# Performance work log

Measured on AMD Instinct MI355X. Metric: run time of the kernel, lower is better.

The kernel has to match this reference:

```python
import jax, jax.numpy as jnp
import numpy as np

T, H, I, E, TOPK = 4096, 1024, 2048, 8, 2
RENORMALIZE = True


def setup_inputs() -> dict:
    key = jax.random.key(0)
    k1, k2, k3, k4 = jax.random.split(key, 4)
    x = jax.random.normal(k1, (T, H), dtype=jnp.float32)
    router_logits = jax.random.normal(k2, (T, E), dtype=jnp.float32)
    # w13 stacks [gate; up] projections: [E, 2*I, H]; w2: [E, H, I]
    w13_weight = jax.random.normal(k3, (E, 2 * I, H), dtype=jnp.float32) * 0.02
    w2_weight = jax.random.normal(k4, (E, H, I), dtype=jnp.float32) * 0.02
    return {
        "x": x,
        "router_logits": router_logits,
        "w13_weight": w13_weight,
        "w2_weight": w2_weight,
        "top_k": TOPK,
    }


def reference(x, router_logits, w13_weight, w2_weight, top_k):
    num_experts = w13_weight.shape[0]
    inter = w13_weight.shape[1] // 2
    # --- routing: softmax -> top-k -> (optional) renormalize ---
    probs = jax.nn.softmax(router_logits, axis=-1)              # [T, E]
    topk_w, topk_ids = jax.lax.top_k(probs, top_k)              # [T, K]
    if RENORMALIZE:
        topk_w = topk_w / jnp.sum(topk_w, axis=-1, keepdims=True)
    topk_w = topk_w.astype(x.dtype)

    # --- grouped expert MLP (SwiGLU): silu(x @ w1.T) * (x @ w3.T) @ w2.T ---
    out = jnp.zeros_like(x)
    for e in range(num_experts):  # fixed small expert count; not a data-dim loop
        coeff = jnp.sum(jnp.where(topk_ids == e, topk_w, 0.0), axis=-1)  # [T]
        w1 = w13_weight[e, :inter, :]   # [I, H]
        w3 = w13_weight[e, inter:, :]   # [I, H]
        gate = x @ w1.T                 # [T, I]
        up = x @ w3.T                   # [T, I]
        h = jax.nn.silu(gate) * up      # [T, I]
        y = h @ w2_weight[e].T          # [T, H]
        out = out + coeff[:, None] * y
    return out
```

## Files before the change

### kernel.cpp

```cpp
#include <hip/hip_runtime.h>

typedef __bf16 bf16x8 __attribute__((ext_vector_type(8)));
typedef float f32x4 __attribute__((ext_vector_type(4)));
typedef unsigned short u16;
typedef unsigned int u32;
typedef u16 u16x8 __attribute__((ext_vector_type(8)));

#define DEVFN static __device__ __forceinline__

constexpr int T = 4096, H = 1024, I = 2048, E = 8;
constexpr int NSLOT = T * 2;
constexpr int BM = 128, BK = 64;
constexpr int BKB = BK * 2;
constexpr int MAX_TILES = 72;

DEVFN u16 f2bf(float f) {
  u32 u = __builtin_bit_cast(u32, f);
  u32 r = (u + 0x7FFFu + ((u >> 16) & 1u)) >> 16;
  return (u16)r;
}

DEVFN void glds16(const void* g, void* l) {
  __builtin_amdgcn_global_load_lds(
      (const __attribute__((address_space(1))) void*)g,
      (__attribute__((address_space(3))) void*)l, 16, 0, 0);
}

__global__ void cvt_f32_bf16(const float* __restrict__ s, u16* __restrict__ d, int n8) {
  int i = blockIdx.x * blockDim.x + threadIdx.x;
  int stride = gridDim.x * blockDim.x;
  for (; i < n8; i += stride) {
    const float4* s4 = (const float4*)s + (size_t)i * 2;
    float4 x0 = s4[0], x1 = s4[1];
    u16x8 o;
    o[0] = f2bf(x0.x); o[1] = f2bf(x0.y); o[2] = f2bf(x0.z); o[3] = f2bf(x0.w);
    o[4] = f2bf(x1.x); o[5] = f2bf(x1.y); o[6] = f2bf(x1.z); o[7] = f2bf(x1.w);
    *((u16x8*)d + i) = o;
  }
}

DEVFN void top2(const float* __restrict__ logits, int t, int& i0, int& i1, float& v0, float& v1) {
  float l[E];
#pragma unroll
  for (int i = 0; i < E; i++) l[i] = logits[t * E + i];
  i0 = 0; v0 = l[0];
#pragma unroll
  for (int i = 1; i < E; i++) if (l[i] > v0) { v0 = l[i]; i0 = i; }
  i1 = -1; v1 = -1e30f;
#pragma unroll
  for (int i = 0; i < E; i++) if (i != i0 && l[i] > v1) { v1 = l[i]; i1 = i; }
}

__global__ void router_count(const float* __restrict__ logits, int* __restrict__ counts) {
  int t = blockIdx.x * blockDim.x + threadIdx.x;
  if (t >= T) return;
  int i0, i1; float v0, v1;
  top2(logits, t, i0, i1, v0, v1);
  atomicAdd(&counts[i0], 1);
  atomicAdd(&counts[i1], 1);
}

__global__ void build_tiles(const int* __restrict__ counts, int* __restrict__ offsets,
                            int* __restrict__ ntiles, int* __restrict__ tile_e,
                            int* __restrict__ tile_r0) {
  if (threadIdx.x != 0 || blockIdx.x != 0) return;
  int s = 0, nt = 0;
  for (int e = 0; e < E; e++) {
    offsets[e] = s;
    for (int r = 0; r < counts[e]; r += BM) { tile_e[nt] = e; tile_r0[nt] = r; nt++; }
    s += counts[e];
  }
  offsets[E] = s;
  ntiles[0] = nt;
}

__global__ void router_scatter(const float* __restrict__ logits, const int* __restrict__ offsets,
                               int* __restrict__ cursor, int* __restrict__ slot_tok,
                               float* __restrict__ slot_w, int* __restrict__ pos) {
  int t = blockIdx.x * blockDim.x + threadIdx.x;
  if (t >= T) return;
  int i0, i1; float v0, v1;
  top2(logits, t, i0, i1, v0, v1);
  float ee = __expf(v1 - v0);
  float w0 = 1.f / (1.f + ee);
  float w1 = 1.f - w0;
  int p0 = offsets[i0] + atomicAdd(&cursor[i0], 1);
  slot_tok[p0] = t; slot_w[p0] = w0; pos[2 * t] = p0;
  int p1 = offsets[i1] + atomicAdd(&cursor[i1], 1);
  slot_tok[p1] = t; slot_w[p1] = w1; pos[2 * t + 1] = p1;
}

__global__ __launch_bounds__(256, 2) void gemm1(
    const u16* __restrict__ xb, const u16* __restrict__ w13b,
    const int* __restrict__ offsets, const int* __restrict__ ntiles,
    const int* __restrict__ tile_e, const int* __restrict__ tile_r0,
    const int* __restrict__ slot_tok, u16* __restrict__ hb) {
  int ti = blockIdx.x;
  if (ti >= ntiles[0]) return;
  int e = tile_e[ti], row0 = tile_r0[ti];
  int n0 = offsets[e], ne = offsets[e + 1] - n0;
  int j0 = blockIdx.y * 128;

  __shared__ u16 As[BM * BK];
  __shared__ u16 Bgs[BM * BK];
  __shared__ u16 Bus[BM * BK];

  int tid = threadIdx.x, w = tid >> 6, l = tid & 63;
  int lr = l & 15, lh = l >> 4;
  int wm = w >> 1, wn = w & 1;

  const char* xc = (const char*)xb;
  const char* wc = (const char*)w13b;

  size_t aoff[4], goff[4], uoff[4];
#pragma unroll
  for (int i = 0; i < 4; i++) {
    int c = tid + i * 256;
    int r = c >> 3;
    int gch = (c & 7) ^ (r & 7);
    int rr = row0 + r; if (rr > ne - 1) rr = ne - 1;
    aoff[i] = (size_t)slot_tok[n0 + rr] * (H * 2) + (size_t)(gch * 16);
    goff[i] = ((size_t)e * (2 * I) + (j0 + r)) * (H * 2) + (size_t)(gch * 16);
    uoff[i] = goff[i] + (size_t)I * (H * 2);
  }

  f32x4 accg[4][4] = {};
  f32x4 accu[4][4] = {};

  char* AsB = (char*)As; char* BgB = (char*)Bgs; char* BuB = (char*)Bus;

  for (int k0 = 0; k0 < H; k0 += BK) {
    __syncthreads();
    size_t kb = (size_t)(k0 * 2);
#pragma unroll
    for (int i = 0; i < 4; i++) {
      int d = (tid + i * 256) * 16;
      glds16(xc + aoff[i] + kb, AsB + d);
      glds16(wc + goff[i] + kb, BgB + d);
      glds16(wc + uoff[i] + kb, BuB + d);
    }
    __syncthreads();

#pragma unroll
    for (int ks = 0; ks < 2; ks++) {
      bf16x8 a[4];
#pragma unroll
      for (int mi = 0; mi < 4; mi++) {
        int row = wm * 64 + mi * 16 + lr;
        a[mi] = *(const bf16x8*)(AsB + row * BKB + (((ks * 4 + lh) ^ (row & 7)) * 16));
      }
#pragma unroll
      for (int ni = 0; ni < 4; ni++) {
        int row = wn * 64 + ni * 16 + lr;
        int boff = row * BKB + (((ks * 4 + lh) ^ (row & 7)) * 16);
        bf16x8 bg = *(const bf16x8*)(BgB + boff);
#pragma unroll
        for (int mi = 0; mi < 4; mi++)
          accg[mi][ni] = __builtin_amdgcn_mfma_f32_16x16x32_bf16(a[mi], bg, accg[mi][ni], 0, 0, 0);
        bf16x8 bu = *(const bf16x8*)(BuB + boff);
#pragma unroll
        for (int mi = 0; mi < 4; mi++)
          accu[mi][ni] = __builtin_amdgcn_mfma_f32_16x16x32_bf16(a[mi], bu, accu[mi][ni], 0, 0, 0);
      }
    }
  }

#pragma unroll
  for (int mi = 0; mi < 4; mi++) {
    int Rb = row0 + wm * 64 + mi * 16 + lh * 4;
#pragma unroll
    for (int ni = 0; ni < 4; ni++) {
      int col = j0 + wn * 64 + ni * 16 + lr;
      f32x4 g = accg[mi][ni], u = accu[mi][ni];
#pragma unroll
      for (int r = 0; r < 4; r++) {
        int R = Rb + r;
        if (R < ne) {
          float gg = g[r];
          float hh = (gg / (1.f + __expf(-gg))) * u[r];
          hb[(size_t)(n0 + R) * I + col] = f2bf(hh);
        }
      }
    }
  }
}

__global__ __launch_bounds__(256, 2) void gemm2(
    const u16* __restrict__ hb, const u16* __restrict__ w2b,
    const int* __restrict__ offsets, const int* __restrict__ ntiles,
    const int* __restrict__ tile_e, const int* __restrict__ tile_r0,
    const float* __restrict__ slot_w, float* __restrict__ ys) {
  int ti = blockIdx.x;
  if (ti >= ntiles[0]) return;
  int e = tile_e[ti], row0 = tile_r0[ti];
  int n0 = offsets[e], ne = offsets[e + 1] - n0;
  int j0 = blockIdx.y * 128;

  __shared__ u16 As[BM * BK];
  __shared__ u16 Bs[BM * BK];

  int tid = threadIdx.x, w = tid >> 6, l = tid & 63;
  int lr = l & 15, lh = l >> 4;
  int wm = w >> 1, wn = w & 1;

  const char* hc = (const char*)hb;
  const char* wc = (const char*)w2b;

  size_t aoff[4], boff[4];
#pragma unroll
  for (int i = 0; i < 4; i++) {
    int c = tid + i * 256;
    int r = c >> 3;
    int gch = (c & 7) ^ (r & 7);
    int rr = row0 + r; if (rr > ne - 1) rr = ne - 1;
    aoff[i] = (size_t)(n0 + rr) * (I * 2) + (size_t)(gch * 16);
    boff[i] = ((size_t)e * H + (j0 + r)) * (I * 2) + (size_t)(gch * 16);
  }

  f32x4 acc[4][4] = {};
  char* AsB = (char*)As; char* BsB = (char*)Bs;

  for (int k0 = 0; k0 < I; k0 += BK) {
    __syncthreads();
    size_t kb = (size_t)(k0 * 2);
#pragma unroll
    for (int i = 0; i < 4; i++) {
      int d = (tid + i * 256) * 16;
      glds16(hc + aoff[i] + kb, AsB + d);
      glds16(wc + boff[i] + kb, BsB + d);
    }
    __syncthreads();

#pragma unroll
    for (int ks = 0; ks < 2; ks++) {
      bf16x8 a[4];
#pragma unroll
      for (int mi = 0; mi < 4; mi++) {
        int row = wm * 64 + mi * 16 + lr;
        a[mi] = *(const bf16x8*)(AsB + row * BKB + (((ks * 4 + lh) ^ (row & 7)) * 16));
      }
#pragma unroll
      for (int nj = 0; nj < 4; nj++) {
        int row = wn * 64 + nj * 16 + lr;
        bf16x8 b = *(const bf16x8*)(BsB + row * BKB + (((ks * 4 + lh) ^ (row & 7)) * 16));
#pragma unroll
        for (int mi = 0; mi < 4; mi++)
          acc[mi][nj] = __builtin_amdgcn_mfma_f32_16x16x32_bf16(a[mi], b, acc[mi][nj], 0, 0, 0);
      }
    }
  }

#pragma unroll
  for (int mi = 0; mi < 4; mi++) {
    int Rb = row0 + wm * 64 + mi * 16 + lh * 4;
#pragma unroll
    for (int r = 0; r < 4; r++) {
      int R = Rb + r;
      if (R < ne) {
        float cw = slot_w[n0 + R];
        float* yrow = ys + (size_t)(n0 + R) * H + j0 + wn * 64 + lr;
#pragma unroll
        for (int nj = 0; nj < 4; nj++)
          yrow[nj * 16] = acc[mi][nj][r] * cw;
      }
    }
  }
}

__global__ void combine(const float* __restrict__ ys, const int* __restrict__ pos,
                        float* __restrict__ out) {
  int idx = blockIdx.x * blockDim.x + threadIdx.x;
  int t = idx >> 8;
  int j = idx & 255;
  int p0 = pos[2 * t], p1 = pos[2 * t + 1];
  const float4* y4 = (const float4*)ys;
  float4 a = y4[(size_t)p0 * 256 + j];
  float4 b = y4[(size_t)p1 * 256 + j];
  float4 o; o.x = a.x + b.x; o.y = a.y + b.y; o.z = a.z + b.z; o.w = a.w + b.w;
  ((float4*)out)[idx] = o;
}

extern "C" void kernel_launch(void* const* d_in, const int* in_sizes, int n_in,
                              void* d_out, int out_size, void* d_ws, size_t ws_size,
                              hipStream_t stream) {
  const float* x      = (const float*)d_in[0];
  const float* logits = (const float*)d_in[1];
  const float* w13    = (const float*)d_in[2];
  const float* w2     = (const float*)d_in[3];
  float* out = (float*)d_out;

  char* ws = (char*)d_ws;
  size_t off = 0;
  auto alloc = [&](size_t b) { size_t p = off; off += (b + 255) & ~(size_t)255; return p; };
  int*   counts   = (int*)(ws + alloc(E * 4));
  int*   cursor   = (int*)(ws + alloc(E * 4));
  int*   offsets  = (int*)(ws + alloc((E + 1) * 4));
  int*   ntiles   = (int*)(ws + alloc(4));
  int*   tile_e   = (int*)(ws + alloc(MAX_TILES * 4));
  int*   tile_r0  = (int*)(ws + alloc(MAX_TILES * 4));
  int*   slot_tok = (int*)(ws + alloc(NSLOT * 4));
  float* slot_w   = (float*)(ws + alloc(NSLOT * 4));
  int*   pos      = (int*)(ws + alloc(2 * T * 4));
  u16*   xb       = (u16*)(ws + alloc((size_t)T * H * 2));
  size_t w13b_off = alloc((size_t)E * 2 * I * H * 2);
  u16*   w13b     = (u16*)(ws + w13b_off);
  u16*   w2b      = (u16*)(ws + alloc((size_t)E * H * I * 2));
  u16*   hb       = (u16*)(ws + alloc((size_t)NSLOT * I * 2));
  float* ys       = (float*)(ws + w13b_off);
  if (ws_size < off) return;

  hipMemsetAsync(ws, 0, 512, stream);

  cvt_f32_bf16<<<2048, 256, 0, stream>>>(x, xb, T * H / 8);
  cvt_f32_bf16<<<2048, 256, 0, stream>>>(w13, w13b, E * 2 * I * H / 8);
  cvt_f32_bf16<<<2048, 256, 0, stream>>>(w2, w2b, E * H * I / 8);

  router_count<<<T / 256, 256, 0, stream>>>(logits, counts);
  build_tiles<<<1, 64, 0, stream>>>(counts, offsets, ntiles, tile_e, tile_r0);
  router_scatter<<<T / 256, 256, 0, stream>>>(logits, offsets, cursor, slot_tok, slot_w, pos);

  gemm1<<<dim3(MAX_TILES, I / 128, 1), 256, 0, stream>>>(
      xb, w13b, offsets, ntiles, tile_e, tile_r0, slot_tok, hb);
  gemm2<<<dim3(MAX_TILES, H / 128, 1), 256, 0, stream>>>(
      hb, w2b, offsets, ntiles, tile_e, tile_r0, slot_w, ys);
  combine<<<T * H / 4 / 256, 256, 0, stream>>>(ys, pos, out);
}
```

Before: 508.1 us.

## Double-buffer GEMM K loop with async LDS loads and fuse prep kernels

Both expert GEMMs now use a BK=32 double-buffered LDS pipeline. The next K slice is issued via global_load_lds before computing on the current one, with explicit vmcnt waits and raw s_barriers in place of the two __syncthreads per step, and the LDS swizzle is adjusted for 64-byte rows. The three conversion kernels are merged into one, and the router count/tile-build/scatter kernels plus the memset are merged into a single-block router kernel using shared-memory atomics, which cuts launch overhead. gemm2 raises its occupancy hint to 3; the single-block router serialises routing work and the smaller K step means more barriers.

Result: no change. 500.3 us (-1.5%).

```diff
diff --git a/kernel.cpp b/kernel.cpp
--- a/kernel.cpp
+++ b/kernel.cpp
@@ -10,8 +10,6 @@
 
 constexpr int T = 4096, H = 1024, I = 2048, E = 8;
 constexpr int NSLOT = T * 2;
-constexpr int BM = 128, BK = 64;
-constexpr int BKB = BK * 2;
 constexpr int MAX_TILES = 72;
 
 DEVFN u16 f2bf(float f) {
@@ -26,10 +24,9 @@
       (__attribute__((address_space(3))) void*)l, 16, 0, 0);
 }
 
-__global__ void cvt_f32_bf16(const float* __restrict__ s, u16* __restrict__ d, int n8) {
-  int i = blockIdx.x * blockDim.x + threadIdx.x;
-  int stride = gridDim.x * blockDim.x;
-  for (; i < n8; i += stride) {
+DEVFN void cvt_region(const float* __restrict__ s, u16* __restrict__ d, int n8,
+                      int id0, int stride) {
+  for (int i = id0; i < n8; i += stride) {
     const float4* s4 = (const float4*)s + (size_t)i * 2;
     float4 x0 = s4[0], x1 = s4[1];
     u16x8 o;
@@ -39,6 +36,16 @@
   }
 }
 
+__global__ void cvt_all(const float* __restrict__ x, const float* __restrict__ w13,
+                        const float* __restrict__ w2, u16* __restrict__ xb,
+                        u16* __restrict__ w13b, u16* __restrict__ w2b) {
+  int id0 = blockIdx.x * blockDim.x + threadIdx.x;
+  int stride = gridDim.x * blockDim.x;
+  cvt_region(x,   xb,   T * H / 8,         id0, stride);
+  cvt_region(w13, w13b, E * 2 * I * H / 8, id0, stride);
+  cvt_region(w2,  w2b,  E * H * I / 8,     id0, stride);
+}
+
 DEVFN void top2(const float* __restrict__ logits, int t, int& i0, int& i1, float& v0, float& v1) {
   float l[E];
 #pragma unroll
@@ -51,43 +58,48 @@
   for (int i = 0; i < E; i++) if (i != i0 && l[i] > v1) { v1 = l[i]; i1 = i; }
 }
 
-__global__ void router_count(const float* __restrict__ logits, int* __restrict__ counts) {
-  int t = blockIdx.x * blockDim.x + threadIdx.x;
-  if (t >= T) return;
-  int i0, i1; float v0, v1;
-  top2(logits, t, i0, i1, v0, v1);
-  atomicAdd(&counts[i0], 1);
-  atomicAdd(&counts[i1], 1);
-}
-
-__global__ void build_tiles(const int* __restrict__ counts, int* __restrict__ offsets,
-                            int* __restrict__ ntiles, int* __restrict__ tile_e,
-                            int* __restrict__ tile_r0) {
-  if (threadIdx.x != 0 || blockIdx.x != 0) return;
-  int s = 0, nt = 0;
-  for (int e = 0; e < E; e++) {
-    offsets[e] = s;
-    for (int r = 0; r < counts[e]; r += BM) { tile_e[nt] = e; tile_r0[nt] = r; nt++; }
-    s += counts[e];
-  }
-  offsets[E] = s;
-  ntiles[0] = nt;
-}
-
-__global__ void router_scatter(const float* __restrict__ logits, const int* __restrict__ offsets,
-                               int* __restrict__ cursor, int* __restrict__ slot_tok,
-                               float* __restrict__ slot_w, int* __restrict__ pos) {
-  int t = blockIdx.x * blockDim.x + threadIdx.x;
-  if (t >= T) return;
-  int i0, i1; float v0, v1;
-  top2(logits, t, i0, i1, v0, v1);
-  float ee = __expf(v1 - v0);
-  float w0 = 1.f / (1.f + ee);
-  float w1 = 1.f - w0;
-  int p0 = offsets[i0] + atomicAdd(&cursor[i0], 1);
-  slot_tok[p0] = t; slot_w[p0] = w0; pos[2 * t] = p0;
-  int p1 = offsets[i1] + atomicAdd(&cursor[i1], 1);
-  slot_tok[p1] = t; slot_w[p1] = w1; pos[2 * t + 1] = p1;
+__global__ void router_all(const float* __restrict__ logits, int* __restrict__ offsets,
+                           int* __restrict__ ntiles, int* __restrict__ tile_e,
+                           int* __restrict__ tile_r0, int* __restrict__ slot_tok,
+                           float* __restrict__ slot_w, int* __restrict__ pos) {
+  __shared__ int cnt[E], cur[E], offs[E + 1];
+  int tid = threadIdx.x;
+  if (tid < E) { cnt[tid] = 0; cur[tid] = 0; }
+  __syncthreads();
+
+  constexpr int PT = T / 256;
+  int e0[PT], e1[PT]; float w0v[PT], w1v[PT];
+#pragma unroll
+  for (int i = 0; i < PT; i++) {
+    int t = tid + i * 256;
+    int i0, i1; float v0, v1;
+    top2(logits, t, i0, i1, v0, v1);
+    float ee = __expf(v1 - v0);
+    float w0 = 1.f / (1.f + ee);
+    e0[i] = i0; e1[i] = i1; w0v[i] = w0; w1v[i] = 1.f - w0;
+    atomicAdd(&cnt[i0], 1);
+    atomicAdd(&cnt[i1], 1);
+  }
+  __syncthreads();
+  if (tid == 0) {
+    int s = 0, nt = 0;
+    for (int e = 0; e < E; e++) {
+      offs[e] = s; offsets[e] = s;
+      for (int r = 0; r < cnt[e]; r += 128) { tile_e[nt] = e; tile_r0[nt] = r; nt++; }
+      s += cnt[e];
+    }
+    offs[E] = s; offsets[E] = s;
+    ntiles[0] = nt;
+  }
+  __syncthreads();
+#pragma unroll
+  for (int i = 0; i < PT; i++) {
+    int t = tid + i * 256;
+    int p0 = offs[e0[i]] + atomicAdd(&cur[e0[i]], 1);
+    slot_tok[p0] = t; slot_w[p0] = w0v[i]; pos[2 * t] = p0;
+    int p1 = offs[e1[i]] + atomicAdd(&cur[e1[i]], 1);
+    slot_tok[p1] = t; slot_w[p1] = w1v[i]; pos[2 * t + 1] = p1;
+  }
 }
 
 __global__ __launch_bounds__(256, 2) void gemm1(
@@ -101,9 +113,10 @@
   int n0 = offsets[e], ne = offsets[e + 1] - n0;
   int j0 = blockIdx.y * 128;
 
-  __shared__ u16 As[BM * BK];
-  __shared__ u16 Bgs[BM * BK];
-  __shared__ u16 Bus[BM * BK];
+  constexpr int TB = 128 * 32;
+  __shared__ u16 As[2 * TB];
+  __shared__ u16 Bgs[2 * TB];
+  __shared__ u16 Bus[2 * TB];
 
   int tid = threadIdx.x, w = tid >> 6, l = tid & 63;
   int lr = l & 15, lh = l >> 4;
@@ -112,57 +125,74 @@
   const char* xc = (const char*)xb;
   const char* wc = (const char*)w13b;
 
-  size_t aoff[4], goff[4], uoff[4];
-#pragma unroll
-  for (int i = 0; i < 4; i++) {
+  size_t aoff[2], goff[2], uoff[2];
+#pragma unroll
+  for (int i = 0; i < 2; i++) {
     int c = tid + i * 256;
-    int r = c >> 3;
-    int gch = (c & 7) ^ (r & 7);
+    int r = c >> 2;
+    int gch = (c & 3) ^ ((r >> 1) & 3);
     int rr = row0 + r; if (rr > ne - 1) rr = ne - 1;
     aoff[i] = (size_t)slot_tok[n0 + rr] * (H * 2) + (size_t)(gch * 16);
     goff[i] = ((size_t)e * (2 * I) + (j0 + r)) * (H * 2) + (size_t)(gch * 16);
     uoff[i] = goff[i] + (size_t)I * (H * 2);
   }
 
+  char* AsB = (char*)As; char* BgB = (char*)Bgs; char* BuB = (char*)Bus;
+
+  auto stage = [&](int buf, int k0) {
+    size_t kb = (size_t)(k0 * 2);
+    char* Ad = AsB + buf * (TB * 2);
+    char* Gd = BgB + buf * (TB * 2);
+    char* Ud = BuB + buf * (TB * 2);
+#pragma unroll
+    for (int i = 0; i < 2; i++) {
+      int d = (tid + i * 256) * 16;
+      glds16(xc + aoff[i] + kb, Ad + d);
+      glds16(wc + goff[i] + kb, Gd + d);
+      glds16(wc + uoff[i] + kb, Ud + d);
+    }
+  };
+
   f32x4 accg[4][4] = {};
   f32x4 accu[4][4] = {};
 
-  char* AsB = (char*)As; char* BgB = (char*)Bgs; char* BuB = (char*)Bus;
-
-  for (int k0 = 0; k0 < H; k0 += BK) {
-    __syncthreads();
-    size_t kb = (size_t)(k0 * 2);
-#pragma unroll
-    for (int i = 0; i < 4; i++) {
-      int d = (tid + i * 256) * 16;
-      glds16(xc + aoff[i] + kb, AsB + d);
-      glds16(wc + goff[i] + kb, BgB + d);
-      glds16(wc + uoff[i] + kb, BuB + d);
-    }
-    __syncthreads();
-
-#pragma unroll
-    for (int ks = 0; ks < 2; ks++) {
-      bf16x8 a[4];
-#pragma unroll
-      for (int mi = 0; mi < 4; mi++) {
-        int row = wm * 64 + mi * 16 + lr;
-        a[mi] = *(const bf16x8*)(AsB + row * BKB + (((ks * 4 + lh) ^ (row & 7)) * 16));
-      }
-#pragma unroll
-      for (int ni = 0; ni < 4; ni++) {
-        int row = wn * 64 + ni * 16 + lr;
-        int boff = row * BKB + (((ks * 4 + lh) ^ (row & 7)) * 16);
-        bf16x8 bg = *(const bf16x8*)(BgB + boff);
-#pragma unroll
-        for (int mi = 0; mi < 4; mi++)
-          accg[mi][ni] = __builtin_amdgcn_mfma_f32_16x16x32_bf16(a[mi], bg, accg[mi][ni], 0, 0, 0);
-        bf16x8 bu = *(const bf16x8*)(BuB + boff);
-#pragma unroll
-        for (int mi = 0; mi < 4; mi++)
-          accu[mi][ni] = __builtin_amdgcn_mfma_f32_16x16x32_bf16(a[mi], bu, accu[mi][ni], 0, 0, 0);
-      }
-    }
+  constexpr int NSTEP = H / 32;
+  stage(0, 0);
+
+  for (int t = 0; t < NSTEP; ++t) {
+    int cb = t & 1;
+    if (t + 1 < NSTEP) {
+      stage(cb ^ 1, (t + 1) * 32);
+      asm volatile("s_waitcnt vmcnt(6)" ::: "memory");
+    } else {
+      asm volatile("s_waitcnt vmcnt(0)" ::: "memory");
+    }
+    __builtin_amdgcn_s_barrier();
+
+    const char* Ab = AsB + cb * (TB * 2);
+    const char* Gb = BgB + cb * (TB * 2);
+    const char* Ub = BuB + cb * (TB * 2);
+    bf16x8 a[4];
+#pragma unroll
+    for (int mi = 0; mi < 4; mi++) {
+      int row = wm * 64 + mi * 16 + lr;
+      a[mi] = *(const bf16x8*)(Ab + row * 64 + ((lh ^ ((row >> 1) & 3)) * 16));
+    }
+#pragma unroll
+    for (int ni = 0; ni < 4; ni++) {
+      int row = wn * 64 + ni * 16 + lr;
+      int boff = row * 64 + ((lh ^ ((row >> 1) & 3)) * 16);
+      bf16x8 bg = *(const bf16x8*)(Gb + boff);
+#pragma unroll
+      for (int mi = 0; mi < 4; mi++)
+        accg[mi][ni] = __builtin_amdgcn_mfma_f32_16x16x32_bf16(a[mi], bg, accg[mi][ni], 0, 0, 0);
+      bf16x8 bu = *(const bf16x8*)(Ub + boff);
+#pragma unroll
+      for (int mi = 0; mi < 4; mi++)
+        accu[mi][ni] = __builtin_amdgcn_mfma_f32_16x16x32_bf16(a[mi], bu, accu[mi][ni], 0, 0, 0);
+    }
+    __builtin_amdgcn_s_barrier();
+    __builtin_amdgcn_sched_barrier(0);
   }
 
 #pragma unroll
@@ -185,7 +215,7 @@
   }
 }
 
-__global__ __launch_bounds__(256, 2) void gemm2(
+__global__ __launch_bounds__(256, 3) void gemm2(
     const u16* __restrict__ hb, const u16* __restrict__ w2b,
     const int* __restrict__ offsets, const int* __restrict__ ntiles,
     const int* __restrict__ tile_e, const int* __restrict__ tile_r0,
@@ -196,8 +226,9 @@
   int n0 = offsets[e], ne = offsets[e + 1] - n0;
   int j0 = blockIdx.y * 128;
 
-  __shared__ u16 As[BM * BK];
-  __shared__ u16 Bs[BM * BK];
+  constexpr int TB = 128 * 32;
+  __shared__ u16 As[2 * TB];
+  __shared__ u16 Bs[2 * TB];
 
   int tid = threadIdx.x, w = tid >> 6, l = tid & 63;
   int lr = l & 15, lh = l >> 4;
@@ -206,48 +237,64 @@
   const char* hc = (const char*)hb;
   const char* wc = (const char*)w2b;
 
-  size_t aoff[4], boff[4];
-#pragma unroll
-  for (int i = 0; i < 4; i++) {
+  size_t aoff[2], boff[2];
+#pragma unroll
+  for (int i = 0; i < 2; i++) {
     int c = tid + i * 256;
-    int r = c >> 3;
-    int gch = (c & 7) ^ (r & 7);
+    int r = c >> 2;
+    int gch = (c & 3) ^ ((r >> 1) & 3);
     int rr = row0 + r; if (rr > ne - 1) rr = ne - 1;
     aoff[i] = (size_t)(n0 + rr) * (I * 2) + (size_t)(gch * 16);
     boff[i] = ((size_t)e * H + (j0 + r)) * (I * 2) + (size_t)(gch * 16);
   }
 
+  char* AsB = (char*)As; char* BsB = (char*)Bs;
+
+  auto stage = [&](int buf, int k0) {
+    size_t kb = (size_t)(k0 * 2);
+    char* Ad = AsB + buf * (TB * 2);
+    char* Bd = BsB + buf * (TB * 2);
+#pragma unroll
+    for (int i = 0; i < 2; i++) {
+      int d = (tid + i * 256) * 16;
+      glds16(hc + aoff[i] + kb, Ad + d);
+      glds16(wc + boff[i] + kb, Bd + d);
+    }
+  };
+
   f32x4 acc[4][4] = {};
-  char* AsB = (char*)As; char* BsB = (char*)Bs;
-
-  for (int k0 = 0; k0 < I; k0 += BK) {
-    __syncthreads();
-    size_t kb = (size_t)(k0 * 2);
-#pragma unroll
-    for (int i = 0; i < 4; i++) {
-      int d = (tid + i * 256) * 16;
-      glds16(hc + aoff[i] + kb, AsB + d);
-      glds16(wc + boff[i] + kb, BsB + d);
-    }
-    __syncthreads();
-
-#pragma unroll
-    for (int ks = 0; ks < 2; ks++) {
-      bf16x8 a[4];
-#pragma unroll
-      for (int mi = 0; mi < 4; mi++) {
-        int row = wm * 64 + mi * 16 + lr;
-        a[mi] = *(const bf16x8*)(AsB + row * BKB + (((ks * 4 + lh) ^ (row & 7)) * 16));
-      }
-#pragma unroll
-      for (int nj = 0; nj < 4; nj++) {
-        int row = wn * 64 + nj * 16 + lr;
-        bf16x8 b = *(const bf16x8*)(BsB + row * BKB + (((ks * 4 + lh) ^ (row & 7)) * 16));
-#pragma unroll
-        for (int mi = 0; mi < 4; mi++)
-          acc[mi][nj] = __builtin_amdgcn_mfma_f32_16x16x32_bf16(a[mi], b, acc[mi][nj], 0, 0, 0);
-      }
-    }
+
+  constexpr int NSTEP = I / 32;
+  stage(0, 0);
+
+  for (int t = 0; t < NSTEP; ++t) {
+    int cb = t & 1;
+    if (t + 1 < NSTEP) {
+      stage(cb ^ 1, (t + 1) * 32);
+      asm volatile("s_waitcnt vmcnt(4)" ::: "memory");
+    } else {
+      asm volatile("s_waitcnt vmcnt(0)" ::: "memory");
+    }
+    __builtin_amdgcn_s_barrier();
+
+    const char* Ab = AsB + cb * (TB * 2);
+    const char* Bb = BsB + cb * (TB * 2);
+    bf16x8 a[4];
+#pragma unroll
+    for (int mi = 0; mi < 4; mi++) {
+      int row = wm * 64 + mi * 16 + lr;
+      a[mi] = *(const bf16x8*)(Ab + row * 64 + ((lh ^ ((row >> 1) & 3)) * 16));
+    }
+#pragma unroll
+    for (int nj = 0; nj < 4; nj++) {
+      int row = wn * 64 + nj * 16 + lr;
+      bf16x8 b = *(const bf16x8*)(Bb + row * 64 + ((lh ^ ((row >> 1) & 3)) * 16));
+#pragma unroll
+      for (int mi = 0; mi < 4; mi++)
+        acc[mi][nj] = __builtin_amdgcn_mfma_f32_16x16x32_bf16(a[mi], b, acc[mi][nj], 0, 0, 0);
+    }
+    __builtin_amdgcn_s_barrier();
+    __builtin_amdgcn_sched_barrier(0);
   }
 
 #pragma unroll
@@ -292,8 +339,6 @@
   char* ws = (char*)d_ws;
   size_t off = 0;
   auto alloc = [&](size_t b) { size_t p = off; off += (b + 255) & ~(size_t)255; return p; };
-  int*   counts   = (int*)(ws + alloc(E * 4));
-  int*   cursor   = (int*)(ws + alloc(E * 4));
   int*   offsets  = (int*)(ws + alloc((E + 1) * 4));
   int*   ntiles   = (int*)(ws + alloc(4));
   int*   tile_e   = (int*)(ws + alloc(MAX_TILES * 4));
@@ -309,16 +354,9 @@
   float* ys       = (float*)(ws + w13b_off);
   if (ws_size < off) return;
 
-  hipMemsetAsync(ws, 0, 512, stream);
-
-  cvt_f32_bf16<<<2048, 256, 0, stream>>>(x, xb, T * H / 8);
-  cvt_f32_bf16<<<2048, 256, 0, stream>>>(w13, w13b, E * 2 * I * H / 8);
-  cvt_f32_bf16<<<2048, 256, 0, stream>>>(w2, w2b, E * H * I / 8);
-
-  router_count<<<T / 256, 256, 0, stream>>>(logits, counts);
-  build_tiles<<<1, 64, 0, stream>>>(counts, offsets, ntiles, tile_e, tile_r0);
-  router_scatter<<<T / 256, 256, 0, stream>>>(logits, offsets, cursor, slot_tok, slot_w, pos);
-
+  cvt_all<<<2048, 256, 0, stream>>>(x, w13, w2, xb, w13b, w2b);
+  router_all<<<1, 256, 0, stream>>>(logits, offsets, ntiles, tile_e, tile_r0,
+                                    slot_tok, slot_w, pos);
   gemm1<<<dim3(MAX_TILES, I / 128, 1), 256, 0, stream>>>(
       xb, w13b, offsets, ntiles, tile_e, tile_r0, slot_tok, hb);
   gemm2<<<dim3(MAX_TILES, H / 128, 1), 256, 0, stream>>>(
```

## Fuse conversions and routing into one kernel; remap GEMM blocks for XCD locality

Applied to the files above, without the earlier changes.

The three fp32-to-bf16 conversion kernels, the memset and the three routing kernels are merged into one launch. An extra block does all routing (top-2, counts, tile build, scatter) using shared-memory atomics. The GEMM grids are flattened to 1D and block indices are remapped so that each of the 8 XCDs handles a contiguous group of 9 row tiles across all column tiles, which should improve L2 reuse of the A tiles. This cuts launch count and serialisation, but the single routing block processes 4096 tokens alone, and slot order within an expert changes.

Result: faster. 431.8 us (-15.0%).

```diff
diff --git a/kernel.cpp b/kernel.cpp
--- a/kernel.cpp
+++ b/kernel.cpp
@@ -26,10 +26,9 @@
       (__attribute__((address_space(3))) void*)l, 16, 0, 0);
 }
 
-__global__ void cvt_f32_bf16(const float* __restrict__ s, u16* __restrict__ d, int n8) {
-  int i = blockIdx.x * blockDim.x + threadIdx.x;
-  int stride = gridDim.x * blockDim.x;
-  for (; i < n8; i += stride) {
+DEVFN void cvt_region(const float* __restrict__ s, u16* __restrict__ d, int n8,
+                      int id0, int stride) {
+  for (int i = id0; i < n8; i += stride) {
     const float4* s4 = (const float4*)s + (size_t)i * 2;
     float4 x0 = s4[0], x1 = s4[1];
     u16x8 o;
@@ -51,43 +50,58 @@
   for (int i = 0; i < E; i++) if (i != i0 && l[i] > v1) { v1 = l[i]; i1 = i; }
 }
 
-__global__ void router_count(const float* __restrict__ logits, int* __restrict__ counts) {
-  int t = blockIdx.x * blockDim.x + threadIdx.x;
-  if (t >= T) return;
-  int i0, i1; float v0, v1;
-  top2(logits, t, i0, i1, v0, v1);
-  atomicAdd(&counts[i0], 1);
-  atomicAdd(&counts[i1], 1);
-}
-
-__global__ void build_tiles(const int* __restrict__ counts, int* __restrict__ offsets,
-                            int* __restrict__ ntiles, int* __restrict__ tile_e,
-                            int* __restrict__ tile_r0) {
-  if (threadIdx.x != 0 || blockIdx.x != 0) return;
-  int s = 0, nt = 0;
-  for (int e = 0; e < E; e++) {
-    offsets[e] = s;
-    for (int r = 0; r < counts[e]; r += BM) { tile_e[nt] = e; tile_r0[nt] = r; nt++; }
-    s += counts[e];
-  }
-  offsets[E] = s;
-  ntiles[0] = nt;
-}
-
-__global__ void router_scatter(const float* __restrict__ logits, const int* __restrict__ offsets,
-                               int* __restrict__ cursor, int* __restrict__ slot_tok,
-                               float* __restrict__ slot_w, int* __restrict__ pos) {
-  int t = blockIdx.x * blockDim.x + threadIdx.x;
-  if (t >= T) return;
-  int i0, i1; float v0, v1;
-  top2(logits, t, i0, i1, v0, v1);
-  float ee = __expf(v1 - v0);
-  float w0 = 1.f / (1.f + ee);
-  float w1 = 1.f - w0;
-  int p0 = offsets[i0] + atomicAdd(&cursor[i0], 1);
-  slot_tok[p0] = t; slot_w[p0] = w0; pos[2 * t] = p0;
-  int p1 = offsets[i1] + atomicAdd(&cursor[i1], 1);
-  slot_tok[p1] = t; slot_w[p1] = w1; pos[2 * t + 1] = p1;
+__global__ void cvt_router(const float* __restrict__ x, const float* __restrict__ w13,
+                           const float* __restrict__ w2, const float* __restrict__ logits,
+                           u16* __restrict__ xb, u16* __restrict__ w13b, u16* __restrict__ w2b,
+                           int* __restrict__ offsets, int* __restrict__ ntiles,
+                           int* __restrict__ tile_e, int* __restrict__ tile_r0,
+                           int* __restrict__ slot_tok, float* __restrict__ slot_w,
+                           int* __restrict__ pos) {
+  if (blockIdx.x == 2048) {
+    __shared__ int cnt[E], cur[E], offs[E + 1];
+    int tid = threadIdx.x;
+    if (tid < E) { cnt[tid] = 0; cur[tid] = 0; }
+    __syncthreads();
+    constexpr int PT = T / 256;
+    int e0[PT], e1[PT]; float w0v[PT], w1v[PT];
+#pragma unroll
+    for (int i = 0; i < PT; i++) {
+      int t = tid + i * 256;
+      int i0, i1; float v0, v1;
+      top2(logits, t, i0, i1, v0, v1);
+      float ee = __expf(v1 - v0);
+      float w0 = 1.f / (1.f + ee);
+      e0[i] = i0; e1[i] = i1; w0v[i] = w0; w1v[i] = 1.f - w0;
+      atomicAdd(&cnt[i0], 1);
+      atomicAdd(&cnt[i1], 1);
+    }
+    __syncthreads();
+    if (tid == 0) {
+      int s = 0, nt = 0;
+      for (int e = 0; e < E; e++) {
+        offs[e] = s; offsets[e] = s;
+        for (int r = 0; r < cnt[e]; r += BM) { tile_e[nt] = e; tile_r0[nt] = r; nt++; }
+        s += cnt[e];
+      }
+      offs[E] = s; offsets[E] = s;
+      ntiles[0] = nt;
+    }
+    __syncthreads();
+#pragma unroll
+    for (int i = 0; i < PT; i++) {
+      int t = tid + i * 256;
+      int p0 = offs[e0[i]] + atomicAdd(&cur[e0[i]], 1);
+      slot_tok[p0] = t; slot_w[p0] = w0v[i]; pos[2 * t] = p0;
+      int p1 = offs[e1[i]] + atomicAdd(&cur[e1[i]], 1);
+      slot_tok[p1] = t; slot_w[p1] = w1v[i]; pos[2 * t + 1] = p1;
+    }
+    return;
+  }
+  int id0 = blockIdx.x * blockDim.x + threadIdx.x;
+  int stride = 2048 * 256;
+  cvt_region(x,   xb,   T * H / 8,         id0, stride);
+  cvt_region(w13, w13b, E * 2 * I * H / 8, id0, stride);
+  cvt_region(w2,  w2b,  E * H * I / 8,     id0, stride);
 }
 
 __global__ __launch_bounds__(256, 2) void gemm1(
@@ -95,11 +109,13 @@
     const int* __restrict__ offsets, const int* __restrict__ ntiles,
     const int* __restrict__ tile_e, const int* __restrict__ tile_r0,
     const int* __restrict__ slot_tok, u16* __restrict__ hb) {
-  int ti = blockIdx.x;
+  int f = blockIdx.x;
+  int xcd = f & 7, idx = f >> 3;
+  int ti = xcd * 9 + (idx % 9);
+  int j0 = (idx / 9) * 128;
   if (ti >= ntiles[0]) return;
   int e = tile_e[ti], row0 = tile_r0[ti];
   int n0 = offsets[e], ne = offsets[e + 1] - n0;
-  int j0 = blockIdx.y * 128;
 
   __shared__ u16 As[BM * BK];
   __shared__ u16 Bgs[BM * BK];
@@ -190,11 +206,13 @@
     const int* __restrict__ offsets, const int* __restrict__ ntiles,
     const int* __restrict__ tile_e, const int* __restrict__ tile_r0,
     const float* __restrict__ slot_w, float* __restrict__ ys) {
-  int ti = blockIdx.x;
+  int f = blockIdx.x;
+  int xcd = f & 7, idx = f >> 3;
+  int ti = xcd * 9 + (idx % 9);
+  int j0 = (idx / 9) * 128;
   if (ti >= ntiles[0]) return;
   int e = tile_e[ti], row0 = tile_r0[ti];
   int n0 = offsets[e], ne = offsets[e + 1] - n0;
-  int j0 = blockIdx.y * 128;
 
   __shared__ u16 As[BM * BK];
   __shared__ u16 Bs[BM * BK];
@@ -292,8 +310,6 @@
   char* ws = (char*)d_ws;
   size_t off = 0;
   auto alloc = [&](size_t b) { size_t p = off; off += (b + 255) & ~(size_t)255; return p; };
-  int*   counts   = (int*)(ws + alloc(E * 4));
-  int*   cursor   = (int*)(ws + alloc(E * 4));
   int*   offsets  = (int*)(ws + alloc((E + 1) * 4));
   int*   ntiles   = (int*)(ws + alloc(4));
   int*   tile_e   = (int*)(ws + alloc(MAX_TILES * 4));
@@ -309,19 +325,12 @@
   float* ys       = (float*)(ws + w13b_off);
   if (ws_size < off) return;
 
-  hipMemsetAsync(ws, 0, 512, stream);
-
-  cvt_f32_bf16<<<2048, 256, 0, stream>>>(x, xb, T * H / 8);
-  cvt_f32_bf16<<<2048, 256, 0, stream>>>(w13, w13b, E * 2 * I * H / 8);
-  cvt_f32_bf16<<<2048, 256, 0, stream>>>(w2, w2b, E * H * I / 8);
-
-  router_count<<<T / 256, 256, 0, stream>>>(logits, counts);
-  build_tiles<<<1, 64, 0, stream>>>(counts, offsets, ntiles, tile_e, tile_r0);
-  router_scatter<<<T / 256, 256, 0, stream>>>(logits, offsets, cursor, slot_tok, slot_w, pos);
-
-  gemm1<<<dim3(MAX_TILES, I / 128, 1), 256, 0, stream>>>(
+  cvt_router<<<2049, 256, 0, stream>>>(x, w13, w2, logits, xb, w13b, w2b,
+                                       offsets, ntiles, tile_e, tile_r0,
+                                       slot_tok, slot_w, pos);
+  gemm1<<<MAX_TILES * (I / 128), 256, 0, stream>>>(
       xb, w13b, offsets, ntiles, tile_e, tile_r0, slot_tok, hb);
-  gemm2<<<dim3(MAX_TILES, H / 128, 1), 256, 0, stream>>>(
+  gemm2<<<MAX_TILES * (H / 128), 256, 0, stream>>>(
       hb, w2b, offsets, ntiles, tile_e, tile_r0, slot_w, ys);
   combine<<<T * H / 4 / 256, 256, 0, stream>>>(ys, pos, out);
 }
```
